# Performance work log

Hardware: AMD Instinct MI355X
Metric: run time of the kernel (lower is better)

## Reference

```python
import jax, jax.numpy as jnp
import numpy as np

NEG_INF = -1e30

def setup_inputs() -> dict:
    key = jax.random.key(0)
    k1, k2, k3, k4, k5 = jax.random.split(key, 5)
    B, N, Fin, Fout, H = 8, 1024, 128, 64, 4
    h = jax.random.normal(k1, (B, N, Fin), dtype=jnp.float32)
    adj = jax.random.randint(k2, (N, N), 0, 2, dtype=jnp.int32)
    bias_matrix = jax.random.normal(k3, (1, 1, N, N), dtype=jnp.float32)
    # xavier-ish scaled params
    W = jax.random.normal(k4, (H, Fin, Fout), dtype=jnp.float32) * (1.0 / np.sqrt(Fin))
    a = jax.random.normal(k5, (H, 2 * Fout, 1), dtype=jnp.float32) * (1.0 / np.sqrt(2 * Fout))
    return {"h": h, "adj": adj, "bias_matrix": bias_matrix, "W": W, "a": a}


def reference(h, adj, bias_matrix, W, a):
    B, N, _ = h.shape
    H, _, Fout = W.shape
    # h_prime: [B, N, H, Fout]
    h_prime = jnp.einsum('bni,hio->bnho', h, W)
    # split attention vector: a_input @ a == h_i @ a1 + h_j @ a2 (same math, no O(N^2*F) tensor)
    a1 = a[:, :Fout, 0]   # [H, Fout]
    a2 = a[:, Fout:, 0]   # [H, Fout]
    ei = jnp.einsum('bnhf,hf->bnh', h_prime, a1)  # [B, N, H]
    ej = jnp.einsum('bnhf,hf->bnh', h_prime, a2)  # [B, N, H]
    e = jax.nn.leaky_relu(ei[:, :, None, :] + ej[:, None, :, :], negative_slope=0.2)  # [B,N,N,H]
    # bias_matrix [1,1,N,N] -> expand to [B,1,N,N] -> permute(0,2,3,1) -> [B,N,N,1]
    bias = jnp.transpose(bias_matrix, (0, 2, 3, 1))  # [1, N, N, 1], broadcasts to [B,N,N,H]
    e = e + bias
    mask = (adj != 0)[None, :, :, None]  # [1, N, N, 1]
    e_masked = jnp.where(mask, e, NEG_INF)
    attention = jax.nn.softmax(e_masked, axis=2)  # softmax over j
    h_out = jnp.einsum('bijh,bjhf->bihf', attention, h_prime)  # [B, N, H, Fout]
    return h_out.reshape(B, N, H * Fout)
```

## Files before the change

### kernel.cpp

```cpp
#include <hip/hip_runtime.h>

constexpr int B = 8, N = 1024, FIN = 128, FOUT = 64, H = 4;
constexpr float LOG2E = 1.44269504f;

typedef __attribute__((ext_vector_type(8))) short short8;
typedef __attribute__((ext_vector_type(4))) short short4v;
typedef __attribute__((ext_vector_type(4))) float f32x4;

static __device__ inline unsigned short f2bf(float x) {
    union { float f; unsigned u; } v; v.f = x;
    unsigned r = v.u + 0x7fff + ((v.u >> 16) & 1);
    return (unsigned short)(r >> 16);
}

__global__ __launch_bounds__(256) void gat_prep(
    const float* __restrict__ h,
    const float* __restrict__ W,
    const float* __restrict__ a,
    const int*   __restrict__ adj,
    const float* __restrict__ bias,
    unsigned short* __restrict__ hpF,
    unsigned short* __restrict__ mbB,
    float* __restrict__ ei_t,
    float* __restrict__ ej_t)
{
    __shared__ float h_lds[8][132];
    const int t = threadIdx.x;

    if (blockIdx.x < 512) {
        const int bx   = blockIdx.x;
        const int ti   = bx >> 3;
        const int jc   = (bx & 7) * 4 + (t >> 6);
        const int lane = t & 63;
        const int i    = ti * 16 + (lane & 15);
        const int j0   = jc * 32 + 8 * (lane >> 4);

        const int4*   ap = reinterpret_cast<const int4*>(adj + (size_t)i * N + j0);
        const float4* bp = reinterpret_cast<const float4*>(bias + (size_t)i * N + j0);
        int4   a0 = ap[0], a1 = ap[1];
        float4 b0 = bp[0], b1 = bp[1];
        unsigned short q0 = f2bf(a0.x ? LOG2E * b0.x : -1e35f);
        unsigned short q1 = f2bf(a0.y ? LOG2E * b0.y : -1e35f);
        unsigned short q2 = f2bf(a0.z ? LOG2E * b0.z : -1e35f);
        unsigned short q3 = f2bf(a0.w ? LOG2E * b0.w : -1e35f);
        unsigned short q4 = f2bf(a1.x ? LOG2E * b1.x : -1e35f);
        unsigned short q5 = f2bf(a1.y ? LOG2E * b1.y : -1e35f);
        unsigned short q6 = f2bf(a1.z ? LOG2E * b1.z : -1e35f);
        unsigned short q7 = f2bf(a1.w ? LOG2E * b1.w : -1e35f);
        int4 ov;
        ov.x = (int)((unsigned)q0 | ((unsigned)q1 << 16));
        ov.y = (int)((unsigned)q2 | ((unsigned)q3 << 16));
        ov.z = (int)((unsigned)q4 | ((unsigned)q5 << 16));
        ov.w = (int)((unsigned)q6 | ((unsigned)q7 << 16));
        *reinterpret_cast<int4*>(mbB + (((size_t)ti * 32 + jc) * 64 + lane) * 8) = ov;
        return;
    }

    const int blk = blockIdx.x - 512;
    const int b   = blk >> 7;
    const int n0  = (blk & 127) * 8;

    {
        const float* src = h + ((size_t)b * N + n0) * FIN;
        float4 x = reinterpret_cast<const float4*>(src)[t];
        int fl = t * 4;
        *reinterpret_cast<float4*>(&h_lds[fl >> 7][fl & 127]) = x;
    }
    __syncthreads();

    const int hd   = t >> 6;
    const int lane = t & 63;
    const int li   = lane & 15;
    const int f0   = li * 4;
    const int g    = (lane >> 4) & 1;
    const int kh   = lane >> 5;

    float acc[4][4];
    #pragma unroll
    for (int k = 0; k < 4; ++k)
        #pragma unroll
        for (int j = 0; j < 4; ++j) acc[k][j] = 0.f;

    const float* Wp = W + (size_t)hd * FIN * FOUT + (size_t)kh * 64 * FOUT + f0;
    #pragma unroll 4
    for (int i = 0; i < 64; ++i) {
        float4 w4 = *reinterpret_cast<const float4*>(Wp + (size_t)i * FOUT);
        #pragma unroll
        for (int k = 0; k < 4; ++k) {
            float hv = h_lds[4 * g + k][kh * 64 + i];
            acc[k][0] = fmaf(hv, w4.x, acc[k][0]);
            acc[k][1] = fmaf(hv, w4.y, acc[k][1]);
            acc[k][2] = fmaf(hv, w4.z, acc[k][2]);
            acc[k][3] = fmaf(hv, w4.w, acc[k][3]);
        }
    }

    #pragma unroll
    for (int k = 0; k < 4; ++k)
        #pragma unroll
        for (int j = 0; j < 4; ++j)
            acc[k][j] += __shfl_xor(acc[k][j], 32, 64);

    const int bh = b * H + hd;
    if (kh == 0) {
        const int jc  = n0 >> 5;
        const int kgp = (n0 >> 3) & 3;
        const int ft  = li >> 2;
        const int e0  = 4 * g;
        #pragma unroll
        for (int jj = 0; jj < 4; ++jj) {
            short4v v4;
            v4[0] = (short)f2bf(acc[0][jj]);
            v4[1] = (short)f2bf(acc[1][jj]);
            v4[2] = (short)f2bf(acc[2][jj]);
            v4[3] = (short)f2bf(acc[3][jj]);
            const int lanep = (4 * (li & 3) + jj) + 16 * kgp;
            *reinterpret_cast<short4v*>(
                hpF + ((((size_t)bh * 32 + jc) * 4 + ft) * 64 + lanep) * 8 + e0) = v4;
        }
    }

    float4 a1 = *reinterpret_cast<const float4*>(a + (size_t)hd * 2 * FOUT + f0);
    float4 a2 = *reinterpret_cast<const float4*>(a + (size_t)hd * 2 * FOUT + FOUT + f0);
    #pragma unroll
    for (int k = 0; k < 4; ++k) {
        float e1 = acc[k][0] * a1.x + acc[k][1] * a1.y + acc[k][2] * a1.z + acc[k][3] * a1.w;
        float e2 = acc[k][0] * a2.x + acc[k][1] * a2.y + acc[k][2] * a2.z + acc[k][3] * a2.w;
        #pragma unroll
        for (int m = 1; m < 16; m <<= 1) {
            e1 += __shfl_xor(e1, m, 64);
            e2 += __shfl_xor(e2, m, 64);
        }
        if ((lane & 15) == 0 && kh == 0) {
            int r = n0 + 4 * g + k;
            ei_t[(size_t)bh * N + r] = LOG2E * e1;
            ej_t[(size_t)bh * N + r] = LOG2E * e2;
        }
    }
}

__global__ __launch_bounds__(512) void gat_attn(
    const unsigned short* __restrict__ hpF,
    const float* __restrict__ ei_t,
    const float* __restrict__ ej_t,
    const unsigned short* __restrict__ mbB,
    float* __restrict__ out)
{
    __shared__ __align__(16) unsigned short hstage[2][2][4][512];
    __shared__ f32x4 red[5][4][64];
    const int raw  = blockIdx.x;
    const int xcd  = raw & 7;
    const int k_   = raw >> 3;
    const int bh   = ((xcd >> 1) << 3) | (k_ >> 3);
    const int it0  = (((xcd & 1) << 3) | (k_ & 7)) * 4;
    const int t    = threadIdx.x;
    const int w8   = t >> 6;
    const int w    = w8 & 3;
    const int jh   = w8 >> 2;
    const int lane = t & 63;
    const int li   = lane & 15;
    const int kg   = lane >> 4;
    const int ti   = it0 + w;
    const int irow = ti * 16 + li;
    const int jcb  = jh * 16;

    const float  ei0   = ei_t[(size_t)bh * N + irow];
    const float* ejrow = ej_t + (size_t)bh * N;
    const unsigned short* mrow = mbB + ((size_t)ti * 32 * 64 + lane) * 8;
    const size_t hbase = (size_t)bh * 65536;

    f32x4 c0 = {0.f,0.f,0.f,0.f}, c1 = {0.f,0.f,0.f,0.f};
    f32x4 c2 = {0.f,0.f,0.f,0.f}, c3 = {0.f,0.f,0.f,0.f};
    f32x4 c4 = {0.f,0.f,0.f,0.f};
    const short obf = (short)0x3F80;
    const short8 ones = {obf,obf,obf,obf,obf,obf,obf,obf};

    #define STAGE(BUF, JCG) {                                                 \
        const unsigned short* gs_ = hpF + hbase + (size_t)(JCG) * 2048        \
                                        + (size_t)w * 512 + (size_t)lane * 8; \
        __builtin_amdgcn_global_load_lds(                                     \
            (const __attribute__((address_space(1))) void*)gs_,               \
            (__attribute__((address_space(3))) void*)&hstage[BUF][jh][w][0],  \
            16, 0, 0); }

    #define DSREAD(BUF, BA, BB, BC, BD) {                                     \
        BA = *reinterpret_cast<const short8*>(&hstage[BUF][jh][0][lane * 8]); \
        BB = *reinterpret_cast<const short8*>(&hstage[BUF][jh][1][lane * 8]); \
        BC = *reinterpret_cast<const short8*>(&hstage[BUF][jh][2][lane * 8]); \
        BD = *reinterpret_cast<const short8*>(&hstage[BUF][jh][3][lane * 8]); }

    #define SCORE2(PL, PH, EJL, EJH, QW) {                                    \
        float bl_ = __uint_as_float(((unsigned)(QW)) << 16);                  \
        float bh_ = __uint_as_float(((unsigned)(QW)) & 0xffff0000u);          \
        float el_ = ei0 + (EJL); el_ = fmaxf(el_, 0.2f * el_) + bl_;          \
        float eh_ = ei0 + (EJH); eh_ = fmaxf(eh_, 0.2f * eh_) + bh_;          \
        asm("v_exp_f32 %0, %1" : "=v"(PL) : "v"(el_));                        \
        asm("v_exp_f32 %0, %1" : "=v"(PH) : "v"(eh_)); }

    #define COMPS(MQ, BA, BB, BC, BD, JC) {                                   \
        float4 ejA = *reinterpret_cast<const float4*>(ejrow + (JC) * 32 + 8 * kg);     \
        float4 ejB = *reinterpret_cast<const float4*>(ejrow + (JC) * 32 + 8 * kg + 4); \
        float p0,p1,p2,p3,p4,p5,p6,p7;                                        \
        SCORE2(p0, p1, ejA.x, ejA.y, MQ.x)                                    \
        SCORE2(p2, p3, ejA.z, ejA.w, MQ.y)                                    \
        SCORE2(p4, p5, ejB.x, ejB.y, MQ.z)                                    \
        SCORE2(p6, p7, ejB.z, ejB.w, MQ.w)                                    \
        int4 pk_;                                                             \
        asm("v_cvt_pk_bf16_f32 %0, %1, %2" : "=v"(pk_.x) : "v"(p0), "v"(p1)); \
        asm("v_cvt_pk_bf16_f32 %0, %1, %2" : "=v"(pk_.y) : "v"(p2), "v"(p3)); \
        asm("v_cvt_pk_bf16_f32 %0, %1, %2" : "=v"(pk_.z) : "v"(p4), "v"(p5)); \
        asm("v_cvt_pk_bf16_f32 %0, %1, %2" : "=v"(pk_.w) : "v"(p6), "v"(p7)); \
        short8 a0_ = *reinterpret_cast<short8*>(&pk_);                        \
        c0 = __builtin_amdgcn_mfma_f32_16x16x32_bf16(a0_, BA, c0, 0, 0, 0);   \
        c1 = __builtin_amdgcn_mfma_f32_16x16x32_bf16(a0_, BB, c1, 0, 0, 0);   \
        c2 = __builtin_amdgcn_mfma_f32_16x16x32_bf16(a0_, BC, c2, 0, 0, 0);   \
        c3 = __builtin_amdgcn_mfma_f32_16x16x32_bf16(a0_, BD, c3, 0, 0, 0);   \
        c4 = __builtin_amdgcn_mfma_f32_16x16x32_bf16(a0_, ones, c4, 0, 0, 0); }

    short8 A0, B0, C0, D0, A1, B1, C1, D1;
    int4 mq0, mq1;

    STAGE(0, jcb)
    mq0 = *reinterpret_cast<const int4*>(mrow + (size_t)jcb * 512);
    __syncthreads();

    for (int jc = 0; jc < 16; jc += 2) {
        STAGE(1, jcb + jc + 1)
        mq1 = *reinterpret_cast<const int4*>(mrow + (size_t)(jcb + jc + 1) * 512);
        DSREAD(0, A0, B0, C0, D0)
        COMPS(mq0, A0, B0, C0, D0, jcb + jc)
        __syncthreads();
        if (jc + 2 < 16) {
            STAGE(0, jcb + jc + 2)
            mq0 = *reinterpret_cast<const int4*>(mrow + (size_t)(jcb + jc + 2) * 512);
        }
        DSREAD(1, A1, B1, C1, D1)
        COMPS(mq1, A1, B1, C1, D1, jcb + jc + 1)
        __syncthreads();
    }
    #undef STAGE
    #undef DSREAD
    #undef SCORE2
    #undef COMPS

    if (jh == 1) {
        red[0][w][lane] = c0;
        red[1][w][lane] = c1;
        red[2][w][lane] = c2;
        red[3][w][lane] = c3;
        red[4][w][lane] = c4;
    }
    __syncthreads();
    if (jh == 1) return;

    c0 += red[0][w][lane];
    c1 += red[1][w][lane];
    c2 += red[2][w][lane];
    c3 += red[3][w][lane];
    c4 += red[4][w][lane];

    const int b  = bh >> 2;
    const int hd = bh & 3;
    #pragma unroll
    for (int r = 0; r < 4; ++r) {
        int orow = ti * 16 + 4 * kg + r;
        float inv = 1.0f / c4[r];
        float* ob = out + (((size_t)b * N + orow) * H + hd) * 64 + li;
        ob[0]  = c0[r] * inv;
        ob[16] = c1[r] * inv;
        ob[32] = c2[r] * inv;
        ob[48] = c3[r] * inv;
    }
}

extern "C" void kernel_launch(void* const* d_in, const int* in_sizes, int n_in,
                              void* d_out, int out_size, void* d_ws, size_t ws_size,
                              hipStream_t stream) {
    const float* h    = (const float*)d_in[0];
    const int*   adj  = (const int*)  d_in[1];
    const float* bias = (const float*)d_in[2];
    const float* W    = (const float*)d_in[3];
    const float* a    = (const float*)d_in[4];
    float* out = (float*)d_out;

    char* ws = (char*)d_ws;
    unsigned short* hpF = (unsigned short*)ws;
    unsigned short* mbB = (unsigned short*)(ws + ((size_t)4 << 20));
    float* ei_t = (float*)(ws + ((size_t)6 << 20));
    float* ej_t = ei_t + (size_t)B * H * N;

    gat_prep<<<512 + B * N / 8, 256, 0, stream>>>(h, W, a, adj, bias,
                                                  hpF, mbB, ei_t, ej_t);
    gat_attn<<<B * H * (N / 64), 512, 0, stream>>>(hpF, ei_t, ej_t, mbB, out);
}
```

Before: 38.11 us.

## Triple-buffer attention staging with vmcnt waits and split prep projection finer

The attention kernel moves from double to triple buffering of the h_prime tile in LDS. It replaces __syncthreads with an explicit vmcnt(4) wait plus s_barrier, so global-to-LDS loads for the next two chunks stay in flight across barriers. The mask and ej register loads are also prefetched one step ahead. The prep kernel processes 4 rows per block instead of 8, splitting the K dimension across 4 lane groups with an extra shuffle reduction, which doubles the projection block count. The risks are a hand-tuned vmcnt count that may be wrong for the actual number of outstanding loads, and one redundant restage at the loop tail.

```diff
diff --git a/kernel.cpp b/kernel.cpp
--- a/kernel.cpp
+++ b/kernel.cpp
@@ -24,7 +24,7 @@
     float* __restrict__ ei_t,
     float* __restrict__ ej_t)
 {
-    __shared__ float h_lds[8][132];
+    __shared__ float h_lds[4][132];
     const int t = threadIdx.x;
 
     if (blockIdx.x < 512) {
@@ -57,10 +57,10 @@
     }
 
     const int blk = blockIdx.x - 512;
-    const int b   = blk >> 7;
-    const int n0  = (blk & 127) * 8;
-
-    {
+    const int b   = blk >> 8;
+    const int n0  = (blk & 255) * 4;
+
+    if (t < 128) {
         const float* src = h + ((size_t)b * N + n0) * FIN;
         float4 x = reinterpret_cast<const float4*>(src)[t];
         int fl = t * 4;
@@ -72,8 +72,7 @@
     const int lane = t & 63;
     const int li   = lane & 15;
     const int f0   = li * 4;
-    const int g    = (lane >> 4) & 1;
-    const int kh   = lane >> 5;
+    const int kh   = lane >> 4;
 
     float acc[4][4];
     #pragma unroll
@@ -81,13 +80,13 @@
         #pragma unroll
         for (int j = 0; j < 4; ++j) acc[k][j] = 0.f;
 
-    const float* Wp = W + (size_t)hd * FIN * FOUT + (size_t)kh * 64 * FOUT + f0;
+    const float* Wp = W + (size_t)hd * FIN * FOUT + (size_t)kh * 32 * FOUT + f0;
     #pragma unroll 4
-    for (int i = 0; i < 64; ++i) {
+    for (int i = 0; i < 32; ++i) {
         float4 w4 = *reinterpret_cast<const float4*>(Wp + (size_t)i * FOUT);
         #pragma unroll
         for (int k = 0; k < 4; ++k) {
-            float hv = h_lds[4 * g + k][kh * 64 + i];
+            float hv = h_lds[k][kh * 32 + i];
             acc[k][0] = fmaf(hv, w4.x, acc[k][0]);
             acc[k][1] = fmaf(hv, w4.y, acc[k][1]);
             acc[k][2] = fmaf(hv, w4.z, acc[k][2]);
@@ -98,15 +97,17 @@
     #pragma unroll
     for (int k = 0; k < 4; ++k)
         #pragma unroll
-        for (int j = 0; j < 4; ++j)
+        for (int j = 0; j < 4; ++j) {
+            acc[k][j] += __shfl_xor(acc[k][j], 16, 64);
             acc[k][j] += __shfl_xor(acc[k][j], 32, 64);
+        }
 
     const int bh = b * H + hd;
     if (kh == 0) {
         const int jc  = n0 >> 5;
-        const int kgp = (n0 >> 3) & 3;
+        const int kgn = (n0 >> 3) & 3;
         const int ft  = li >> 2;
-        const int e0  = 4 * g;
+        const int e0  = n0 & 4;
         #pragma unroll
         for (int jj = 0; jj < 4; ++jj) {
             short4v v4;
@@ -114,7 +115,7 @@
             v4[1] = (short)f2bf(acc[1][jj]);
             v4[2] = (short)f2bf(acc[2][jj]);
             v4[3] = (short)f2bf(acc[3][jj]);
-            const int lanep = (4 * (li & 3) + jj) + 16 * kgp;
+            const int lanep = (4 * (li & 3) + jj) + 16 * kgn;
             *reinterpret_cast<short4v*>(
                 hpF + ((((size_t)bh * 32 + jc) * 4 + ft) * 64 + lanep) * 8 + e0) = v4;
         }
@@ -131,8 +132,8 @@
             e1 += __shfl_xor(e1, m, 64);
             e2 += __shfl_xor(e2, m, 64);
         }
-        if ((lane & 15) == 0 && kh == 0) {
-            int r = n0 + 4 * g + k;
+        if (lane == 0) {
+            int r = n0 + k;
             ei_t[(size_t)bh * N + r] = LOG2E * e1;
             ej_t[(size_t)bh * N + r] = LOG2E * e2;
         }
@@ -146,7 +147,7 @@
     const unsigned short* __restrict__ mbB,
     float* __restrict__ out)
 {
-    __shared__ __align__(16) unsigned short hstage[2][2][4][512];
+    __shared__ __align__(16) unsigned short hstage[3][2][4][512];
     __shared__ f32x4 red[5][4][64];
     const int raw  = blockIdx.x;
     const int xcd  = raw & 7;
@@ -175,6 +176,9 @@
     const short obf = (short)0x3F80;
     const short8 ones = {obf,obf,obf,obf,obf,obf,obf,obf};
 
+    #define VMCNT4() asm volatile("s_waitcnt vmcnt(4)" ::: "memory")
+    #define BARRIER() { __builtin_amdgcn_s_barrier(); asm volatile("" ::: "memory"); }
+
     #define STAGE(BUF, JCG) {                                                 \
         const unsigned short* gs_ = hpF + hbase + (size_t)(JCG) * 2048        \
                                         + (size_t)w * 512 + (size_t)lane * 8; \
@@ -183,6 +187,11 @@
             (__attribute__((address_space(3))) void*)&hstage[BUF][jh][w][0],  \
             16, 0, 0); }
 
+    #define REGS(S, JCG) {                                                    \
+        mq##S  = *reinterpret_cast<const int4*>(mrow + (size_t)(JCG) * 512);  \
+        ejA##S = *reinterpret_cast<const float4*>(ejrow + (JCG) * 32 + 8 * kg);\
+        ejB##S = *reinterpret_cast<const float4*>(ejrow + (JCG) * 32 + 8 * kg + 4); }
+
     #define DSREAD(BUF, BA, BB, BC, BD) {                                     \
         BA = *reinterpret_cast<const short8*>(&hstage[BUF][jh][0][lane * 8]); \
         BB = *reinterpret_cast<const short8*>(&hstage[BUF][jh][1][lane * 8]); \
@@ -197,14 +206,12 @@
         asm("v_exp_f32 %0, %1" : "=v"(PL) : "v"(el_));                        \
         asm("v_exp_f32 %0, %1" : "=v"(PH) : "v"(eh_)); }
 
-    #define COMPS(MQ, BA, BB, BC, BD, JC) {                                   \
-        float4 ejA = *reinterpret_cast<const float4*>(ejrow + (JC) * 32 + 8 * kg);     \
-        float4 ejB = *reinterpret_cast<const float4*>(ejrow + (JC) * 32 + 8 * kg + 4); \
+    #define COMPS(S, BA, BB, BC, BD) {                                        \
         float p0,p1,p2,p3,p4,p5,p6,p7;                                        \
-        SCORE2(p0, p1, ejA.x, ejA.y, MQ.x)                                    \
-        SCORE2(p2, p3, ejA.z, ejA.w, MQ.y)                                    \
-        SCORE2(p4, p5, ejB.x, ejB.y, MQ.z)                                    \
-        SCORE2(p6, p7, ejB.z, ejB.w, MQ.w)                                    \
+        SCORE2(p0, p1, ejA##S.x, ejA##S.y, mq##S.x)                           \
+        SCORE2(p2, p3, ejA##S.z, ejA##S.w, mq##S.y)                           \
+        SCORE2(p4, p5, ejB##S.x, ejB##S.y, mq##S.z)                           \
+        SCORE2(p6, p7, ejB##S.z, ejB##S.w, mq##S.w)                           \
         int4 pk_;                                                             \
         asm("v_cvt_pk_bf16_f32 %0, %1, %2" : "=v"(pk_.x) : "v"(p0), "v"(p1)); \
         asm("v_cvt_pk_bf16_f32 %0, %1, %2" : "=v"(pk_.y) : "v"(p2), "v"(p3)); \
@@ -219,26 +226,39 @@
 
     short8 A0, B0, C0, D0, A1, B1, C1, D1;
     int4 mq0, mq1;
-
-    STAGE(0, jcb)
-    mq0 = *reinterpret_cast<const int4*>(mrow + (size_t)jcb * 512);
-    __syncthreads();
-
-    for (int jc = 0; jc < 16; jc += 2) {
-        STAGE(1, jcb + jc + 1)
-        mq1 = *reinterpret_cast<const int4*>(mrow + (size_t)(jcb + jc + 1) * 512);
-        DSREAD(0, A0, B0, C0, D0)
-        COMPS(mq0, A0, B0, C0, D0, jcb + jc)
-        __syncthreads();
-        if (jc + 2 < 16) {
-            STAGE(0, jcb + jc + 2)
-            mq0 = *reinterpret_cast<const int4*>(mrow + (size_t)(jcb + jc + 2) * 512);
-        }
-        DSREAD(1, A1, B1, C1, D1)
-        COMPS(mq1, A1, B1, C1, D1, jcb + jc + 1)
-        __syncthreads();
-    }
+    float4 ejA0, ejB0, ejA1, ejB1;
+
+    STAGE(0, jcb + 0)
+    STAGE(1, jcb + 1)
+    REGS(0, jcb + 0)
+    VMCNT4();
+    BARRIER();
+
+    int ba = 0, bb = 1;
+    #pragma unroll 1
+    for (int k = 0; k < 16; k += 2) {
+        const int p2 = (k + 2 < 16) ? jcb + k + 2 : jcb + 15;
+        const int p3 = (k + 3 < 16) ? jcb + k + 3 : jcb + 15;
+        const int bn0 = ba == 0 ? 2 : (ba == 1 ? 0 : 1);
+        const int bn1 = bb == 0 ? 2 : (bb == 1 ? 0 : 1);
+        STAGE(bn0, p2)
+        REGS(1, jcb + k + 1)
+        DSREAD(ba, A0, B0, C0, D0)
+        COMPS(0, A0, B0, C0, D0)
+        VMCNT4();
+        BARRIER();
+        STAGE(bn1, p3)
+        REGS(0, p2)
+        DSREAD(bb, A1, B1, C1, D1)
+        COMPS(1, A1, B1, C1, D1)
+        VMCNT4();
+        BARRIER();
+        ba = bn0; bb = bn1;
+    }
+    #undef VMCNT4
+    #undef BARRIER
     #undef STAGE
+    #undef REGS
     #undef DSREAD
     #undef SCORE2
     #undef COMPS
@@ -289,7 +309,7 @@
     float* ei_t = (float*)(ws + ((size_t)6 << 20));
     float* ej_t = ei_t + (size_t)B * H * N;
 
-    gat_prep<<<512 + B * N / 8, 256, 0, stream>>>(h, W, a, adj, bias,
+    gat_prep<<<512 + B * N / 4, 256, 0, stream>>>(h, W, a, adj, bias,
                                                   hpF, mbB, ei_t, ej_t);
     gat_attn<<<B * H * (N / 64), 512, 0, stream>>>(hpF, ei_t, ej_t, mbB, out);
 }
```

Result: slower. 42.64 us (+11.9%).
